# Kernel tuning notes

Hardware: AMD Instinct MI355X
Metric: run time of the kernel (lower is better)

The kernel has to match this reference:

```python
import jax, jax.numpy as jnp
import numpy as np

N_HEAD = 12

def setup_inputs() -> dict:
    key = jax.random.key(0)
    ks = jax.random.split(key, 5)
    B, T, C = 2, 2048, 768
    s = 0.02
    return {
        "x": jax.random.normal(ks[0], (B, T, C), jnp.float32),
        "c_attn_w": jax.random.normal(ks[1], (C, 3 * C), jnp.float32) * s,
        "c_attn_b": jax.random.normal(ks[2], (3 * C,), jnp.float32) * s,
        "c_proj_w": jax.random.normal(ks[3], (C, C), jnp.float32) * s,
        "c_proj_b": jax.random.normal(ks[4], (C,), jnp.float32) * s,
    }

def reference(x, c_attn_w, c_attn_b, c_proj_w, c_proj_b):
    B, T, C = x.shape
    H = N_HEAD
    D = C // H
    qkv = x @ c_attn_w + c_attn_b              # [B,T,3C]
    q, k, v = jnp.split(qkv, 3, axis=-1)
    # [B,T,C] -> [B,H,T,D]
    q = q.reshape(B, T, H, D).transpose(0, 2, 1, 3)
    k = k.reshape(B, T, H, D).transpose(0, 2, 1, 3)
    v = v.reshape(B, T, H, D).transpose(0, 2, 1, 3)
    att = jnp.einsum('bhqd,bhkd->bhqk', q, k) * (1.0 / np.sqrt(D))
    causal = jnp.tril(jnp.ones((T, T), bool))  # [T,T]
    att = jnp.where(causal[None, None], att, jnp.float32(-jnp.inf))
    att = jax.nn.softmax(att, axis=-1)
    y = jnp.einsum('bhqk,bhkd->bhqd', att, v)  # [B,H,T,D]
    y = y.transpose(0, 2, 1, 3).reshape(B, T, C)
    return y @ c_proj_w + c_proj_b
```

## Files before the change

### kernel.cpp

```cpp
#include <hip/hip_runtime.h>
#include <hip/hip_bf16.h>


using half4   = __attribute__((ext_vector_type(4))) _Float16;
using half8   = __attribute__((ext_vector_type(8))) _Float16;
using floatx4 = __attribute__((ext_vector_type(4))) float;

#define T_SEQ 2048
#define NHEAD 12
#define HDIM 64
#define C3 2304
#define CDIM 768
#define BT 4096
#define BH 24

static __device__ inline _Float16 f2h(float f) { return (_Float16)f; }

__global__ __launch_bounds__(256)
void prologue(const float* __restrict__ x, const float* __restrict__ wa,
              const float* __restrict__ wp, _Float16* __restrict__ xb,
              _Float16* __restrict__ wTa, _Float16* __restrict__ wTp) {
    __shared__ float tile[32][33];
    int blk = blockIdx.x, tid = threadIdx.x;
    if (blk < 2304) {
        const float* w; _Float16* wT; int K, N, bx, by;
        if (blk < 1728) { w = wa; wT = wTa; K = CDIM; N = C3; bx = blk % 72; by = blk / 72; }
        else { int b2 = blk - 1728; w = wp; wT = wTp; K = CDIM; N = CDIM; bx = b2 % 24; by = b2 / 24; }
        int tx = tid & 31, ty = tid >> 5;
        #pragma unroll
        for (int j = 0; j < 32; j += 8) {
            int k = by * 32 + ty + j, n = bx * 32 + tx;
            tile[ty + j][tx] = w[(long)k * N + n];
        }
        __syncthreads();
        #pragma unroll
        for (int j = 0; j < 32; j += 8) {
            int nO = bx * 32 + ty + j, kO = by * 32 + tx;
            wT[(long)nO * K + kO] = f2h(tile[tx][ty + j]);
        }
    } else {
        int b2 = blk - 2304;
        long e0 = (long)b2 * 4096 + tid * 16;
        floatx4 f0 = *(const floatx4*)&x[e0];
        floatx4 f1 = *(const floatx4*)&x[e0 + 4];
        floatx4 f2 = *(const floatx4*)&x[e0 + 8];
        floatx4 f3 = *(const floatx4*)&x[e0 + 12];
        half8 h0, h1;
        #pragma unroll
        for (int j = 0; j < 4; ++j) {
            h0[j] = f2h(f0[j]); h0[4 + j] = f2h(f1[j]);
            h1[j] = f2h(f2[j]); h1[4 + j] = f2h(f3[j]);
        }
        *(half8*)&xb[e0] = h0;
        *(half8*)&xb[e0 + 8] = h1;
    }
}

__global__ __launch_bounds__(256)
void gemm_qkv(const _Float16* __restrict__ A, const _Float16* __restrict__ Bt,
              const float* __restrict__ bias,
              _Float16* __restrict__ Qb, _Float16* __restrict__ Kb,
              _Float16* __restrict__ Vt) {
    __shared__ __align__(16) _Float16 As[128 * 72];
    __shared__ __align__(16) _Float16 Bs[96 * 72];
    const int K = CDIM;
    int tid = threadIdx.x;
    int m0 = blockIdx.x * 128, n0 = blockIdx.y * 96;
    int w = tid >> 6, l = tid & 63;
    int wm = (w >> 1) * 64, wn = (w & 1) * 48;
    int lr = l & 15, lq = l >> 4;

    int rs = tid >> 3, cs = (tid & 7) * 8;

    floatx4 acc[4][3] = {};

    half8 Ar[4], Br[3];
    #pragma unroll
    for (int j = 0; j < 4; ++j)
        Ar[j] = *(const half8*)&A[(long)(m0 + j * 32 + rs) * K + cs];
    #pragma unroll
    for (int j = 0; j < 3; ++j)
        Br[j] = *(const half8*)&Bt[(long)(n0 + j * 32 + rs) * K + cs];

    for (int kb = 0; kb < K; kb += 64) {
        #pragma unroll
        for (int j = 0; j < 4; ++j)
            *(half8*)&As[(j * 32 + rs) * 72 + cs] = Ar[j];
        #pragma unroll
        for (int j = 0; j < 3; ++j)
            *(half8*)&Bs[(j * 32 + rs) * 72 + cs] = Br[j];
        __syncthreads();
        if (kb + 64 < K) {
            #pragma unroll
            for (int j = 0; j < 4; ++j)
                Ar[j] = *(const half8*)&A[(long)(m0 + j * 32 + rs) * K + kb + 64 + cs];
            #pragma unroll
            for (int j = 0; j < 3; ++j)
                Br[j] = *(const half8*)&Bt[(long)(n0 + j * 32 + rs) * K + kb + 64 + cs];
        }
        #pragma unroll
        for (int kh = 0; kh < 2; ++kh) {
            half8 af[4], bf[3];
            #pragma unroll
            for (int i = 0; i < 4; ++i)
                af[i] = *(const half8*)&As[(wm + i * 16 + lr) * 72 + kh * 32 + lq * 8];
            #pragma unroll
            for (int i = 0; i < 3; ++i)
                bf[i] = *(const half8*)&Bs[(wn + i * 16 + lr) * 72 + kh * 32 + lq * 8];
            #pragma unroll
            for (int mi = 0; mi < 4; ++mi)
                #pragma unroll
                for (int ni = 0; ni < 3; ++ni)
                    acc[mi][ni] = __builtin_amdgcn_mfma_f32_16x16x32_f16(af[mi], bf[ni], acc[mi][ni], 0, 0, 0);
        }
        __syncthreads();
    }

    int region = n0 / CDIM;
    if (region < 2) {
        _Float16* O = region ? Kb : Qb;
        int nc0 = n0 - region * CDIM + wn;
        #pragma unroll
        for (int mi = 0; mi < 4; ++mi)
            #pragma unroll
            for (int ni = 0; ni < 3; ++ni) {
                int col = nc0 + ni * 16 + lr;
                float bsc = bias[region * CDIM + col];
                #pragma unroll
                for (int r = 0; r < 4; ++r) {
                    int row = m0 + wm + mi * 16 + lq * 4 + r;
                    O[(long)row * CDIM + col] = f2h(acc[mi][ni][r] + bsc);
                }
            }
    } else {
        #pragma unroll
        for (int mi = 0; mi < 4; ++mi)
            #pragma unroll
            for (int ni = 0; ni < 3; ++ni) {
                int cv = n0 - 2 * CDIM + wn + ni * 16 + lr;
                float bsc = bias[2 * CDIM + cv];
                int h = cv >> 6, d = cv & 63;
                int t0 = m0 + wm + mi * 16 + lq * 4;
                int bb = t0 >> 11, t = t0 & 2047;
                half4 hv;
                #pragma unroll
                for (int r = 0; r < 4; ++r) hv[r] = f2h(acc[mi][ni][r] + bsc);
                *(half4*)&Vt[(((long)bb * NHEAD + h) * HDIM + d) * T_SEQ + t] = hv;
            }
    }
}

__global__ __launch_bounds__(256)
void gemm_proj(const _Float16* __restrict__ A, const _Float16* __restrict__ Bt,
               const float* __restrict__ bias, float* __restrict__ Cout) {
    __shared__ __align__(16) _Float16 As[64 * 72];
    __shared__ __align__(16) _Float16 Bs[96 * 72];
    const int K = CDIM, N = CDIM;
    int tid = threadIdx.x;
    int m0 = blockIdx.x * 64, n0 = blockIdx.y * 96;
    int w = tid >> 6, l = tid & 63;
    int wm = (w >> 1) * 32, wn = (w & 1) * 48;
    int lr = l & 15, lq = l >> 4;

    int rs = tid >> 3, cs = (tid & 7) * 8;

    floatx4 acc[2][3] = {};

    half8 Ar[2], Br[3];
    #pragma unroll
    for (int j = 0; j < 2; ++j)
        Ar[j] = *(const half8*)&A[(long)(m0 + j * 32 + rs) * K + cs];
    #pragma unroll
    for (int j = 0; j < 3; ++j)
        Br[j] = *(const half8*)&Bt[(long)(n0 + j * 32 + rs) * K + cs];

    for (int kb = 0; kb < K; kb += 64) {
        #pragma unroll
        for (int j = 0; j < 2; ++j)
            *(half8*)&As[(j * 32 + rs) * 72 + cs] = Ar[j];
        #pragma unroll
        for (int j = 0; j < 3; ++j)
            *(half8*)&Bs[(j * 32 + rs) * 72 + cs] = Br[j];
        __syncthreads();
        if (kb + 64 < K) {
            #pragma unroll
            for (int j = 0; j < 2; ++j)
                Ar[j] = *(const half8*)&A[(long)(m0 + j * 32 + rs) * K + kb + 64 + cs];
            #pragma unroll
            for (int j = 0; j < 3; ++j)
                Br[j] = *(const half8*)&Bt[(long)(n0 + j * 32 + rs) * K + kb + 64 + cs];
        }
        #pragma unroll
        for (int kh = 0; kh < 2; ++kh) {
            half8 af[2], bf[3];
            #pragma unroll
            for (int i = 0; i < 2; ++i)
                af[i] = *(const half8*)&As[(wm + i * 16 + lr) * 72 + kh * 32 + lq * 8];
            #pragma unroll
            for (int i = 0; i < 3; ++i)
                bf[i] = *(const half8*)&Bs[(wn + i * 16 + lr) * 72 + kh * 32 + lq * 8];
            #pragma unroll
            for (int mi = 0; mi < 2; ++mi)
                #pragma unroll
                for (int ni = 0; ni < 3; ++ni)
                    acc[mi][ni] = __builtin_amdgcn_mfma_f32_16x16x32_f16(af[mi], bf[ni], acc[mi][ni], 0, 0, 0);
        }
        __syncthreads();
    }
    #pragma unroll
    for (int mi = 0; mi < 2; ++mi)
        #pragma unroll
        for (int ni = 0; ni < 3; ++ni) {
            int col = n0 + wn + ni * 16 + lr;
            float b = bias[col];
            #pragma unroll
            for (int r = 0; r < 4; ++r) {
                int row = m0 + wm + mi * 16 + lq * 4 + r;
                Cout[(long)row * N + col] = acc[mi][ni][r] + b;
            }
        }
}

__global__ __launch_bounds__(256)
void attn_kernel(const _Float16* __restrict__ Qb, const _Float16* __restrict__ Kb,
                 const _Float16* __restrict__ Vt, _Float16* __restrict__ y) {
    __shared__ __align__(16) _Float16 Ks[128 * 72];
    __shared__ __align__(16) _Float16 Vs[64 * 136];
    __shared__ __align__(16) _Float16 Ps[4][16 * 136];
    int tid = threadIdx.x;
    int w = tid >> 6, l = tid & 63;
    int lr = l & 15, lq = l >> 4;
    int i = blockIdx.x;
    int round = i >> 8, c = i & 255;
    int r_ = (round == 0) ? c : (round == 1 ? 767 - c : 256 + c);
    int qb = 31 - r_ / 24;
    int bh = r_ % 24;
    int b = bh / NHEAD, h = bh % NHEAD;
    int q0 = qb * 64 + w * 16;

    const _Float16* Qp = Qb + (long)b * T_SEQ * CDIM + h * HDIM;
    const _Float16* Kg = Kb + (long)b * T_SEQ * CDIM + h * HDIM;
    const _Float16* Vg = Vt + (long)bh * HDIM * T_SEQ;

    int kr = tid >> 3, kc = (tid & 7) * 8;
    int vr = tid >> 4, vc = (tid & 15) * 8;

    const float qscale = 0.125f * 1.44269504f;
    half8 aq[2];
    #pragma unroll
    for (int kk = 0; kk < 2; ++kk) {
        aq[kk] = *(const half8*)&Qp[(long)(q0 + lr) * CDIM + kk * 32 + lq * 8];
        #pragma unroll
        for (int j = 0; j < 8; ++j) aq[kk][j] = f2h((float)aq[kk][j] * qscale);
    }

    int nk = (qb + 2) >> 1;

    half8 Kr[4], Vr[4];
    #pragma unroll
    for (int j = 0; j < 4; ++j) {
        Kr[j] = *(const half8*)&Kg[(long)(j * 32 + kr) * CDIM + kc];
        Vr[j] = *(const half8*)&Vg[(long)(j * 16 + vr) * T_SEQ + vc];
    }

    float psum = 0.f;
    floatx4 acc[4] = {};
    int qrow = q0 + lr;

    for (int kt = 0; kt < nk; ++kt) {
        int kbase = kt * 128;
        #pragma unroll
        for (int j = 0; j < 4; ++j) {
            *(half8*)&Ks[(j * 32 + kr) * 72 + kc] = Kr[j];
            *(half8*)&Vs[(j * 16 + vr) * 136 + vc] = Vr[j];
        }
        __syncthreads();
        if (kt + 1 < nk) {
            int nb = kbase + 128;
            #pragma unroll
            for (int j = 0; j < 4; ++j) {
                Kr[j] = *(const half8*)&Kg[(long)(nb + j * 32 + kr) * CDIM + kc];
                Vr[j] = *(const half8*)&Vg[(long)(j * 16 + vr) * T_SEQ + nb + vc];
            }
        }

        floatx4 sacc[8];
        #pragma unroll
        for (int s = 0; s < 8; ++s) sacc[s] = floatx4{0.f, 0.f, 0.f, 0.f};
        #pragma unroll
        for (int s = 0; s < 8; ++s)
            #pragma unroll
            for (int kh = 0; kh < 2; ++kh) {
                half8 bk = *(const half8*)&Ks[(s * 16 + lr) * 72 + kh * 32 + lq * 8];
                sacc[s] = __builtin_amdgcn_mfma_f32_16x16x32_f16(bk, aq[kh], sacc[s], 0, 0, 0);
            }

        if (kt == nk - 1) {
            #pragma unroll
            for (int s = 0; s < 8; ++s) {
                half4 hv;
                #pragma unroll
                for (int r = 0; r < 4; ++r) {
                    int key = kbase + s * 16 + lq * 4 + r;
                    float p = (key > qrow) ? 0.f : __builtin_amdgcn_exp2f(sacc[s][r]);
                    psum += p;
                    hv[r] = f2h(p);
                }
                *(half4*)&Ps[w][lr * 136 + s * 16 + lq * 4] = hv;
            }
        } else {
            #pragma unroll
            for (int s = 0; s < 8; ++s) {
                half4 hv;
                #pragma unroll
                for (int r = 0; r < 4; ++r) {
                    float p = __builtin_amdgcn_exp2f(sacc[s][r]);
                    psum += p;
                    hv[r] = f2h(p);
                }
                *(half4*)&Ps[w][lr * 136 + s * 16 + lq * 4] = hv;
            }
        }

        half8 ap[4];
        #pragma unroll
        for (int kk = 0; kk < 4; ++kk)
            ap[kk] = *(const half8*)&Ps[w][lr * 136 + kk * 32 + lq * 8];
        #pragma unroll
        for (int n = 0; n < 4; ++n) {
            #pragma unroll
            for (int kk = 0; kk < 4; ++kk) {
                half8 bv = *(const half8*)&Vs[(n * 16 + lr) * 136 + kk * 32 + lq * 8];
                acc[n] = __builtin_amdgcn_mfma_f32_16x16x32_f16(ap[kk], bv, acc[n], 0, 0, 0);
            }
        }
        __syncthreads();
    }

    float L = psum;
    L += __shfl_xor(L, 16, 64);
    L += __shfl_xor(L, 32, 64);
    float Lr[4];
    #pragma unroll
    for (int r = 0; r < 4; ++r) Lr[r] = __shfl(L, lq * 4 + r, 64);

    #pragma unroll
    for (int n = 0; n < 4; ++n)
        #pragma unroll
        for (int r = 0; r < 4; ++r) {
            int row = q0 + lq * 4 + r;
            float v = acc[n][r] / Lr[r];
            y[((long)(b * T_SEQ) + row) * CDIM + h * HDIM + n * 16 + lr] = f2h(v);
        }
}

extern "C" void kernel_launch(void* const* d_in, const int* in_sizes, int n_in,
                              void* d_out, int out_size, void* d_ws, size_t ws_size,
                              hipStream_t stream) {
    const float* x      = (const float*)d_in[0];
    const float* w_attn = (const float*)d_in[1];
    const float* b_attn = (const float*)d_in[2];
    const float* w_proj = (const float*)d_in[3];
    const float* b_proj = (const float*)d_in[4];
    float* out = (float*)d_out;

    char* ws = (char*)d_ws;
    _Float16* xb  = (_Float16*)(ws);
    _Float16* wTa = (_Float16*)(ws + 6291456);
    _Float16* wTp = (_Float16*)(ws + 9830400);
    _Float16* Qb  = (_Float16*)(ws + 11010048);
    _Float16* Kb  = (_Float16*)(ws + 17301504);
    _Float16* Vt  = (_Float16*)(ws + 23592960);
    _Float16* yb  = (_Float16*)(ws + 29884416);

    prologue<<<3072, 256, 0, stream>>>(x, w_attn, w_proj, xb, wTa, wTp);

    gemm_qkv<<<dim3(BT / 128, C3 / 96), 256, 0, stream>>>(xb, wTa, b_attn, Qb, Kb, Vt);

    attn_kernel<<<BH * (T_SEQ / 64), 256, 0, stream>>>(Qb, Kb, Vt, yb);

    gemm_proj<<<dim3(BT / 64, CDIM / 96), 256, 0, stream>>>(yb, wTp, b_proj, out);
}
```

Baseline: 142.1 us.

## Load GEMM tiles directly into LDS and widen QKV tile to 128x128

Both projection GEMMs now fill shared memory with global_load_lds 16-byte direct-to-LDS loads instead of staging through registers and then storing. This removes the register round-trip and frees VGPRs. It also drops the register prefetch of the next K slice and the row padding, so global loads are no longer overlapped with MFMA work inside a block, and unpadded 128-byte rows may cause LDS bank conflicts on the fragment reads. The QKV GEMM tile grows from 128x96 to 128x128 with 4x4 MFMA accumulators per wave, giving more reuse per block but fewer blocks in the grid.

```diff
diff --git a/kernel.cpp b/kernel.cpp
--- a/kernel.cpp
+++ b/kernel.cpp
@@ -15,6 +15,12 @@
 #define BH 24
 
 static __device__ inline _Float16 f2h(float f) { return (_Float16)f; }
+
+static __device__ inline void gload16(const _Float16* g, _Float16* s) {
+    __builtin_amdgcn_global_load_lds(
+        (const __attribute__((address_space(1))) void*)g,
+        (__attribute__((address_space(3))) void*)s, 16, 0, 0);
+}
 
 __global__ __launch_bounds__(256)
 void prologue(const float* __restrict__ x, const float* __restrict__ wa,
@@ -61,70 +67,59 @@
               const float* __restrict__ bias,
               _Float16* __restrict__ Qb, _Float16* __restrict__ Kb,
               _Float16* __restrict__ Vt) {
-    __shared__ __align__(16) _Float16 As[128 * 72];
-    __shared__ __align__(16) _Float16 Bs[96 * 72];
+    __shared__ __align__(16) _Float16 As[128 * 64];
+    __shared__ __align__(16) _Float16 Bs[128 * 64];
     const int K = CDIM;
     int tid = threadIdx.x;
-    int m0 = blockIdx.x * 128, n0 = blockIdx.y * 96;
+    int m0 = blockIdx.x * 128, n0 = blockIdx.y * 128;
     int w = tid >> 6, l = tid & 63;
-    int wm = (w >> 1) * 64, wn = (w & 1) * 48;
+    int wm = (w >> 1) * 64, wn = (w & 1) * 64;
     int lr = l & 15, lq = l >> 4;
 
-    int rs = tid >> 3, cs = (tid & 7) * 8;
-
-    floatx4 acc[4][3] = {};
-
-    half8 Ar[4], Br[3];
-    #pragma unroll
-    for (int j = 0; j < 4; ++j)
-        Ar[j] = *(const half8*)&A[(long)(m0 + j * 32 + rs) * K + cs];
-    #pragma unroll
-    for (int j = 0; j < 3; ++j)
-        Br[j] = *(const half8*)&Bt[(long)(n0 + j * 32 + rs) * K + cs];
+    int srow = w * 8 + (l >> 3);
+    int scol = (l & 7) * 8;
+    const _Float16* ag = A + (long)(m0 + srow) * K + scol;
+    const _Float16* bg = Bt + (long)(n0 + srow) * K + scol;
+    _Float16* as = &As[srow * 64 + scol];
+    _Float16* bs = &Bs[srow * 64 + scol];
+
+    floatx4 acc[4][4] = {};
 
     for (int kb = 0; kb < K; kb += 64) {
         #pragma unroll
         for (int j = 0; j < 4; ++j)
-            *(half8*)&As[(j * 32 + rs) * 72 + cs] = Ar[j];
-        #pragma unroll
-        for (int j = 0; j < 3; ++j)
-            *(half8*)&Bs[(j * 32 + rs) * 72 + cs] = Br[j];
-        __syncthreads();
-        if (kb + 64 < K) {
-            #pragma unroll
-            for (int j = 0; j < 4; ++j)
-                Ar[j] = *(const half8*)&A[(long)(m0 + j * 32 + rs) * K + kb + 64 + cs];
-            #pragma unroll
-            for (int j = 0; j < 3; ++j)
-                Br[j] = *(const half8*)&Bt[(long)(n0 + j * 32 + rs) * K + kb + 64 + cs];
-        }
+            gload16(ag + (long)j * 32 * K + kb, as + j * 32 * 64);
+        #pragma unroll
+        for (int j = 0; j < 4; ++j)
+            gload16(bg + (long)j * 32 * K + kb, bs + j * 32 * 64);
+        __syncthreads();
         #pragma unroll
         for (int kh = 0; kh < 2; ++kh) {
-            half8 af[4], bf[3];
+            half8 af[4], bf[4];
             #pragma unroll
             for (int i = 0; i < 4; ++i)
-                af[i] = *(const half8*)&As[(wm + i * 16 + lr) * 72 + kh * 32 + lq * 8];
-            #pragma unroll
-            for (int i = 0; i < 3; ++i)
-                bf[i] = *(const half8*)&Bs[(wn + i * 16 + lr) * 72 + kh * 32 + lq * 8];
+                af[i] = *(const half8*)&As[(wm + i * 16 + lr) * 64 + kh * 32 + lq * 8];
+            #pragma unroll
+            for (int i = 0; i < 4; ++i)
+                bf[i] = *(const half8*)&Bs[(wn + i * 16 + lr) * 64 + kh * 32 + lq * 8];
             #pragma unroll
             for (int mi = 0; mi < 4; ++mi)
                 #pragma unroll
-                for (int ni = 0; ni < 3; ++ni)
+                for (int ni = 0; ni < 4; ++ni)
                     acc[mi][ni] = __builtin_amdgcn_mfma_f32_16x16x32_f16(af[mi], bf[ni], acc[mi][ni], 0, 0, 0);
         }
         __syncthreads();
     }
 
-    int region = n0 / CDIM;
+    int region = blockIdx.y / 6;
+    int nr = (blockIdx.y % 6) * 128;
     if (region < 2) {
         _Float16* O = region ? Kb : Qb;
-        int nc0 = n0 - region * CDIM + wn;
         #pragma unroll
         for (int mi = 0; mi < 4; ++mi)
             #pragma unroll
-            for (int ni = 0; ni < 3; ++ni) {
-                int col = nc0 + ni * 16 + lr;
+            for (int ni = 0; ni < 4; ++ni) {
+                int col = nr + wn + ni * 16 + lr;
                 float bsc = bias[region * CDIM + col];
                 #pragma unroll
                 for (int r = 0; r < 4; ++r) {
@@ -136,8 +131,8 @@
         #pragma unroll
         for (int mi = 0; mi < 4; ++mi)
             #pragma unroll
-            for (int ni = 0; ni < 3; ++ni) {
-                int cv = n0 - 2 * CDIM + wn + ni * 16 + lr;
+            for (int ni = 0; ni < 4; ++ni) {
+                int cv = nr + wn + ni * 16 + lr;
                 float bsc = bias[2 * CDIM + cv];
                 int h = cv >> 6, d = cv & 63;
                 int t0 = m0 + wm + mi * 16 + lq * 4;
@@ -153,8 +148,8 @@
 __global__ __launch_bounds__(256)
 void gemm_proj(const _Float16* __restrict__ A, const _Float16* __restrict__ Bt,
                const float* __restrict__ bias, float* __restrict__ Cout) {
-    __shared__ __align__(16) _Float16 As[64 * 72];
-    __shared__ __align__(16) _Float16 Bs[96 * 72];
+    __shared__ __align__(16) _Float16 As[64 * 64];
+    __shared__ __align__(16) _Float16 Bs[96 * 64];
     const int K = CDIM, N = CDIM;
     int tid = threadIdx.x;
     int m0 = blockIdx.x * 64, n0 = blockIdx.y * 96;
@@ -162,43 +157,32 @@
     int wm = (w >> 1) * 32, wn = (w & 1) * 48;
     int lr = l & 15, lq = l >> 4;
 
-    int rs = tid >> 3, cs = (tid & 7) * 8;
+    int srow = w * 8 + (l >> 3);
+    int scol = (l & 7) * 8;
+    const _Float16* ag = A + (long)(m0 + srow) * K + scol;
+    const _Float16* bg = Bt + (long)(n0 + srow) * K + scol;
+    _Float16* as = &As[srow * 64 + scol];
+    _Float16* bs = &Bs[srow * 64 + scol];
 
     floatx4 acc[2][3] = {};
 
-    half8 Ar[2], Br[3];
-    #pragma unroll
-    for (int j = 0; j < 2; ++j)
-        Ar[j] = *(const half8*)&A[(long)(m0 + j * 32 + rs) * K + cs];
-    #pragma unroll
-    for (int j = 0; j < 3; ++j)
-        Br[j] = *(const half8*)&Bt[(long)(n0 + j * 32 + rs) * K + cs];
-
     for (int kb = 0; kb < K; kb += 64) {
         #pragma unroll
         for (int j = 0; j < 2; ++j)
-            *(half8*)&As[(j * 32 + rs) * 72 + cs] = Ar[j];
+            gload16(ag + (long)j * 32 * K + kb, as + j * 32 * 64);
         #pragma unroll
         for (int j = 0; j < 3; ++j)
-            *(half8*)&Bs[(j * 32 + rs) * 72 + cs] = Br[j];
-        __syncthreads();
-        if (kb + 64 < K) {
-            #pragma unroll
-            for (int j = 0; j < 2; ++j)
-                Ar[j] = *(const half8*)&A[(long)(m0 + j * 32 + rs) * K + kb + 64 + cs];
-            #pragma unroll
-            for (int j = 0; j < 3; ++j)
-                Br[j] = *(const half8*)&Bt[(long)(n0 + j * 32 + rs) * K + kb + 64 + cs];
-        }
+            gload16(bg + (long)j * 32 * K + kb, bs + j * 32 * 64);
+        __syncthreads();
         #pragma unroll
         for (int kh = 0; kh < 2; ++kh) {
             half8 af[2], bf[3];
             #pragma unroll
             for (int i = 0; i < 2; ++i)
-                af[i] = *(const half8*)&As[(wm + i * 16 + lr) * 72 + kh * 32 + lq * 8];
+                af[i] = *(const half8*)&As[(wm + i * 16 + lr) * 64 + kh * 32 + lq * 8];
             #pragma unroll
             for (int i = 0; i < 3; ++i)
-                bf[i] = *(const half8*)&Bs[(wn + i * 16 + lr) * 72 + kh * 32 + lq * 8];
+                bf[i] = *(const half8*)&Bs[(wn + i * 16 + lr) * 64 + kh * 32 + lq * 8];
             #pragma unroll
             for (int mi = 0; mi < 2; ++mi)
                 #pragma unroll
@@ -375,7 +359,7 @@
 
     prologue<<<3072, 256, 0, stream>>>(x, w_attn, w_proj, xb, wTa, wTp);
 
-    gemm_qkv<<<dim3(BT / 128, C3 / 96), 256, 0, stream>>>(xb, wTa, b_attn, Qb, Kb, Vt);
+    gemm_qkv<<<dim3(BT / 128, C3 / 128), 256, 0, stream>>>(xb, wTa, b_attn, Qb, Kb, Vt);
 
     attn_kernel<<<BH * (T_SEQ / 64), 256, 0, stream>>>(Qb, Kb, Vt, yb);
 
```

Result: slower. 158.0 us (+11.2%).

## Give each attention wave 32 query rows with two waves per block

Applied to the files above, without the earlier changes.

The attention block shrinks from four waves of 16 query rows to two waves of 32 rows, keeping 64 queries per block. Each K fragment and V fragment read from LDS now feeds two MFMAs, which halves shared-memory read traffic per unit of matrix work. Each thread now issues twice as many global loads to stage the K/V tiles. The trade-off is fewer waves per block at roughly the same LDS footprint, which lowers resident waves per CU and leaves less room to hide latency, while register pressure also rises.

```diff
diff --git a/kernel.cpp b/kernel.cpp
--- a/kernel.cpp
+++ b/kernel.cpp
@@ -221,12 +221,12 @@
         }
 }
 
-__global__ __launch_bounds__(256)
+__global__ __launch_bounds__(128)
 void attn_kernel(const _Float16* __restrict__ Qb, const _Float16* __restrict__ Kb,
                  const _Float16* __restrict__ Vt, _Float16* __restrict__ y) {
     __shared__ __align__(16) _Float16 Ks[128 * 72];
     __shared__ __align__(16) _Float16 Vs[64 * 136];
-    __shared__ __align__(16) _Float16 Ps[4][16 * 136];
+    __shared__ __align__(16) _Float16 Ps[2][32 * 136];
     int tid = threadIdx.x;
     int w = tid >> 6, l = tid & 63;
     int lr = l & 15, lq = l >> 4;
@@ -236,7 +236,7 @@
     int qb = 31 - r_ / 24;
     int bh = r_ % 24;
     int b = bh / NHEAD, h = bh % NHEAD;
-    int q0 = qb * 64 + w * 16;
+    int q0w = qb * 64 + w * 32;
 
     const _Float16* Qp = Qb + (long)b * T_SEQ * CDIM + h * HDIM;
     const _Float16* Kg = Kb + (long)b * T_SEQ * CDIM + h * HDIM;
@@ -246,112 +246,127 @@
     int vr = tid >> 4, vc = (tid & 15) * 8;
 
     const float qscale = 0.125f * 1.44269504f;
-    half8 aq[2];
-    #pragma unroll
-    for (int kk = 0; kk < 2; ++kk) {
-        aq[kk] = *(const half8*)&Qp[(long)(q0 + lr) * CDIM + kk * 32 + lq * 8];
-        #pragma unroll
-        for (int j = 0; j < 8; ++j) aq[kk][j] = f2h((float)aq[kk][j] * qscale);
-    }
+    half8 aq[2][2];
+    #pragma unroll
+    for (int s2 = 0; s2 < 2; ++s2)
+        #pragma unroll
+        for (int kk = 0; kk < 2; ++kk) {
+            aq[s2][kk] = *(const half8*)&Qp[(long)(q0w + s2 * 16 + lr) * CDIM + kk * 32 + lq * 8];
+            #pragma unroll
+            for (int j = 0; j < 8; ++j) aq[s2][kk][j] = f2h((float)aq[s2][kk][j] * qscale);
+        }
 
     int nk = (qb + 2) >> 1;
 
-    half8 Kr[4], Vr[4];
-    #pragma unroll
-    for (int j = 0; j < 4; ++j) {
-        Kr[j] = *(const half8*)&Kg[(long)(j * 32 + kr) * CDIM + kc];
-        Vr[j] = *(const half8*)&Vg[(long)(j * 16 + vr) * T_SEQ + vc];
-    }
-
-    float psum = 0.f;
-    floatx4 acc[4] = {};
-    int qrow = q0 + lr;
+    half8 Kr[8], Vr[8];
+    #pragma unroll
+    for (int j = 0; j < 8; ++j) {
+        Kr[j] = *(const half8*)&Kg[(long)(j * 16 + kr) * CDIM + kc];
+        Vr[j] = *(const half8*)&Vg[(long)(j * 8 + vr) * T_SEQ + vc];
+    }
+
+    float psum[2] = {0.f, 0.f};
+    floatx4 acc[4][2] = {};
+    int qrow0 = q0w + lr, qrow1 = q0w + 16 + lr;
 
     for (int kt = 0; kt < nk; ++kt) {
         int kbase = kt * 128;
         #pragma unroll
-        for (int j = 0; j < 4; ++j) {
-            *(half8*)&Ks[(j * 32 + kr) * 72 + kc] = Kr[j];
-            *(half8*)&Vs[(j * 16 + vr) * 136 + vc] = Vr[j];
+        for (int j = 0; j < 8; ++j) {
+            *(half8*)&Ks[(j * 16 + kr) * 72 + kc] = Kr[j];
+            *(half8*)&Vs[(j * 8 + vr) * 136 + vc] = Vr[j];
         }
         __syncthreads();
         if (kt + 1 < nk) {
             int nb = kbase + 128;
             #pragma unroll
-            for (int j = 0; j < 4; ++j) {
-                Kr[j] = *(const half8*)&Kg[(long)(nb + j * 32 + kr) * CDIM + kc];
-                Vr[j] = *(const half8*)&Vg[(long)(j * 16 + vr) * T_SEQ + nb + vc];
-            }
-        }
-
-        floatx4 sacc[8];
-        #pragma unroll
-        for (int s = 0; s < 8; ++s) sacc[s] = floatx4{0.f, 0.f, 0.f, 0.f};
+            for (int j = 0; j < 8; ++j) {
+                Kr[j] = *(const half8*)&Kg[(long)(nb + j * 16 + kr) * CDIM + kc];
+                Vr[j] = *(const half8*)&Vg[(long)(j * 8 + vr) * T_SEQ + nb + vc];
+            }
+        }
+
+        floatx4 sacc[8][2];
         #pragma unroll
         for (int s = 0; s < 8; ++s)
+            #pragma unroll
+            for (int s2 = 0; s2 < 2; ++s2) sacc[s][s2] = floatx4{0.f, 0.f, 0.f, 0.f};
+        #pragma unroll
+        for (int s = 0; s < 8; ++s) {
             #pragma unroll
             for (int kh = 0; kh < 2; ++kh) {
                 half8 bk = *(const half8*)&Ks[(s * 16 + lr) * 72 + kh * 32 + lq * 8];
-                sacc[s] = __builtin_amdgcn_mfma_f32_16x16x32_f16(bk, aq[kh], sacc[s], 0, 0, 0);
-            }
+                sacc[s][0] = __builtin_amdgcn_mfma_f32_16x16x32_f16(bk, aq[0][kh], sacc[s][0], 0, 0, 0);
+                sacc[s][1] = __builtin_amdgcn_mfma_f32_16x16x32_f16(bk, aq[1][kh], sacc[s][1], 0, 0, 0);
+            }
+        }
 
         if (kt == nk - 1) {
             #pragma unroll
             for (int s = 0; s < 8; ++s) {
-                half4 hv;
+                half4 hv0, hv1;
                 #pragma unroll
                 for (int r = 0; r < 4; ++r) {
                     int key = kbase + s * 16 + lq * 4 + r;
-                    float p = (key > qrow) ? 0.f : __builtin_amdgcn_exp2f(sacc[s][r]);
-                    psum += p;
-                    hv[r] = f2h(p);
+                    float p0 = (key > qrow0) ? 0.f : __builtin_amdgcn_exp2f(sacc[s][0][r]);
+                    float p1 = (key > qrow1) ? 0.f : __builtin_amdgcn_exp2f(sacc[s][1][r]);
+                    psum[0] += p0; psum[1] += p1;
+                    hv0[r] = f2h(p0); hv1[r] = f2h(p1);
                 }
-                *(half4*)&Ps[w][lr * 136 + s * 16 + lq * 4] = hv;
+                *(half4*)&Ps[w][(lr) * 136 + s * 16 + lq * 4] = hv0;
+                *(half4*)&Ps[w][(16 + lr) * 136 + s * 16 + lq * 4] = hv1;
             }
         } else {
             #pragma unroll
             for (int s = 0; s < 8; ++s) {
-                half4 hv;
+                half4 hv0, hv1;
                 #pragma unroll
                 for (int r = 0; r < 4; ++r) {
-                    float p = __builtin_amdgcn_exp2f(sacc[s][r]);
-                    psum += p;
-                    hv[r] = f2h(p);
+                    float p0 = __builtin_amdgcn_exp2f(sacc[s][0][r]);
+                    float p1 = __builtin_amdgcn_exp2f(sacc[s][1][r]);
+                    psum[0] += p0; psum[1] += p1;
+                    hv0[r] = f2h(p0); hv1[r] = f2h(p1);
                 }
-                *(half4*)&Ps[w][lr * 136 + s * 16 + lq * 4] = hv;
-            }
-        }
-
-        half8 ap[4];
-        #pragma unroll
-        for (int kk = 0; kk < 4; ++kk)
-            ap[kk] = *(const half8*)&Ps[w][lr * 136 + kk * 32 + lq * 8];
+                *(half4*)&Ps[w][(lr) * 136 + s * 16 + lq * 4] = hv0;
+                *(half4*)&Ps[w][(16 + lr) * 136 + s * 16 + lq * 4] = hv1;
+            }
+        }
+
+        half8 ap[2][4];
+        #pragma unroll
+        for (int s2 = 0; s2 < 2; ++s2)
+            #pragma unroll
+            for (int kk = 0; kk < 4; ++kk)
+                ap[s2][kk] = *(const half8*)&Ps[w][(s2 * 16 + lr) * 136 + kk * 32 + lq * 8];
         #pragma unroll
         for (int n = 0; n < 4; ++n) {
             #pragma unroll
             for (int kk = 0; kk < 4; ++kk) {
                 half8 bv = *(const half8*)&Vs[(n * 16 + lr) * 136 + kk * 32 + lq * 8];
-                acc[n] = __builtin_amdgcn_mfma_f32_16x16x32_f16(ap[kk], bv, acc[n], 0, 0, 0);
-            }
-        }
-        __syncthreads();
-    }
-
-    float L = psum;
-    L += __shfl_xor(L, 16, 64);
-    L += __shfl_xor(L, 32, 64);
-    float Lr[4];
-    #pragma unroll
-    for (int r = 0; r < 4; ++r) Lr[r] = __shfl(L, lq * 4 + r, 64);
-
-    #pragma unroll
-    for (int n = 0; n < 4; ++n)
-        #pragma unroll
-        for (int r = 0; r < 4; ++r) {
-            int row = q0 + lq * 4 + r;
-            float v = acc[n][r] / Lr[r];
-            y[((long)(b * T_SEQ) + row) * CDIM + h * HDIM + n * 16 + lr] = f2h(v);
-        }
+                acc[n][0] = __builtin_amdgcn_mfma_f32_16x16x32_f16(ap[0][kk], bv, acc[n][0], 0, 0, 0);
+                acc[n][1] = __builtin_amdgcn_mfma_f32_16x16x32_f16(ap[1][kk], bv, acc[n][1], 0, 0, 0);
+            }
+        }
+        __syncthreads();
+    }
+
+    #pragma unroll
+    for (int s2 = 0; s2 < 2; ++s2) {
+        float L = psum[s2];
+        L += __shfl_xor(L, 16, 64);
+        L += __shfl_xor(L, 32, 64);
+        float Lr[4];
+        #pragma unroll
+        for (int r = 0; r < 4; ++r) Lr[r] = __shfl(L, lq * 4 + r, 64);
+        #pragma unroll
+        for (int n = 0; n < 4; ++n)
+            #pragma unroll
+            for (int r = 0; r < 4; ++r) {
+                int row = q0w + s2 * 16 + lq * 4 + r;
+                float v = acc[n][s2][r] / Lr[r];
+                y[((long)(b * T_SEQ) + row) * CDIM + h * HDIM + n * 16 + lr] = f2h(v);
+            }
+    }
 }
 
 extern "C" void kernel_launch(void* const* d_in, const int* in_sizes, int n_in,
@@ -377,7 +392,7 @@
 
     gemm_qkv<<<dim3(BT / 128, C3 / 96), 256, 0, stream>>>(xb, wTa, b_attn, Qb, Kb, Vt);
 
-    attn_kernel<<<BH * (T_SEQ / 64), 256, 0, stream>>>(Qb, Kb, Vt, yb);
+    attn_kernel<<<BH * (T_SEQ / 64), 128, 0, stream>>>(Qb, Kb, Vt, yb);
 
     gemm_proj<<<dim3(BT / 64, CDIM / 96), 256, 0, stream>>>(yb, wTp, b_proj, out);
 }
```

After: 141.8 us. Within noise of the previous version (-0.2%).
